# Kernel tuning notes

Hardware: AMD Instinct MI355X
Metric: run time of the kernel (lower is better)

Reference implementation:

```python
import jax, jax.numpy as jnp
from jax import lax
import numpy as np

BOX_SIZE = 64      # box_size
KERNEL = 5         # maxpool kernel (pad=2, stride=1)
THRESH = 0.95
MAX_BOXES = 256    # fixed-shape cap replacing torch nonzero()
NEG = -1e30        # padding value standing in for 'outside the image'


def setup_inputs() -> dict:
    key = jax.random.key(0)
    k1, k2 = jax.random.split(key)
    category_grids = jax.random.uniform(k1, (8, 3, 256, 256), dtype=jnp.float32)
    images = jax.random.normal(k2, (8, 3, 1024, 1024), dtype=jnp.float32)
    return {"category_grids": category_grids, "images": images}


def _maxpool_same(x):
    # nn.MaxPool2d(kernel_size=5, padding=2, stride=1)
    return lax.reduce_window(x, -jnp.inf, lax.max,
                             (1, 1, KERNEL, KERNEL), (1, 1, 1, 1), 'SAME')


def reference(category_grids, images):
    B, C, Hg, Wg = category_grids.shape
    # ---- GridsToBoxes: maxpool-equality peak NMS + threshold ----
    is_peak = (_maxpool_same(category_grids) == category_grids) & (category_grids > THRESH)
    peaks = category_grids * is_peak  # zero everywhere except peaks

    # fixed-shape replacement for nonzero(): per-image top-k over (C*Hg*Wg)
    flat = peaks.reshape(B, -1)
    vals, idx = lax.top_k(flat, MAX_BOXES)          # [B, K]
    valid = vals > 0.0                              # peak values are > THRESH > 0
    rem = idx % (Hg * Wg)
    cy = rem // Wg                                  # [B, K] int32
    cx = rem % Wg

    half = BOX_SIZE // 2
    x1 = cx - half
    y1 = cy - half
    # box_convert cxcywh -> xyxy
    boxes = jnp.stack([x1, y1, cx + half, cy + half], axis=-1).astype(jnp.float32)  # [B,K,4]

    # ---- CenterCrop: roi_pool(images, boxes, output_size=BOX_SIZE) ----
    # torchvision roi_pool: roi_width = x2-x1+1 = BOX_SIZE+1, adaptive max-pooled to BOX_SIZE bins;
    # out-of-image bins give 0. Emulate by padding with NEG and max-gathering fixed bins.
    P = BOX_SIZE + 1
    pad = BOX_SIZE
    padded = jnp.pad(images, ((0, 0), (0, 0), (pad, pad), (pad, pad)),
                     constant_values=NEG)

    def crop_one(img, y, x):  # img: [3, Hp, Wp]
        return lax.dynamic_slice(img, (0, y + pad, x + pad), (img.shape[0], P, P))

    patches = jax.vmap(lambda img, ys, xs:
                       jax.vmap(lambda y, x: crop_one(img, y, x))(ys, xs)
                       )(padded, y1, x1)            # [B, K, 3, P, P]

    # static adaptive-maxpool bin boundaries: bin i covers [floor(i*P/O), ceil((i+1)*P/O))
    O = BOX_SIZE
    i = np.arange(O)
    b0 = np.floor(i * P / O).astype(np.int32)       # bin width is 1 or 2 -> two gathers suffice
    b1 = (np.ceil((i + 1) * P / O) - 1).astype(np.int32)
    rows = jnp.maximum(patches[..., b0, :], patches[..., b1, :])   # pool H: [B,K,3,O,P]
    pooled = jnp.maximum(rows[..., b0], rows[..., b1])             # pool W: [B,K,3,O,O]
    pooled = jnp.where(pooled < NEG * 0.5, 0.0, pooled)            # empty/outside bins -> 0
    pooled = pooled * valid[:, :, None, None, None].astype(pooled.dtype)

    return peaks, boxes, pooled, valid
```

## Files before the change

kernel.cpp:

```cpp
#include <hip/hip_runtime.h>
#include <stdint.h>
#include <math.h>

#define NB 8
#define NC 3
#define HG 256
#define WG 256
#define IMG 1024
#define TOPK 256
#define HALF 32
#define PEAK_THRESH 0.95f
#define NEGV (-1e30f)
#define SELCAP 2048
#define VB_LO 0x3F733334u
#define NBUCK 256
#define BSHIFT 12

#define ROWS_PB 16
#define GRPS (HG / ROWS_PB)
#define PLANES (NB * NC)
#define PK_BLOCKS (PLANES * GRPS)
#define SLOTS 256

#define PROWS 65
#define PQUADS 17
#define PSTRIDE 76

typedef float f32x4 __attribute__((ext_vector_type(4)));

#define WS_BCAND_OFF 4096
#define WS_SEL_OFF   (WS_BCAND_OFF + (size_t)PK_BLOCKS * SLOTS * 8)

__global__ void __launch_bounds__(256) peaks_kernel(const float* __restrict__ g,
                                                    float* __restrict__ peaks_out,
                                                    uint32_t* __restrict__ bcnt,
                                                    unsigned long long* __restrict__ bcand) {
    __shared__ float vms[ROWS_PB][WG];
    __shared__ unsigned long long lkeys[SLOTS];
    __shared__ uint32_t lcount;

    int blk   = blockIdx.x;
    int grp   = blk & (GRPS - 1);
    int plane = blk >> 4;
    int c     = plane % NC;
    int y0    = grp * ROWS_PB;
    int x     = threadIdx.x;

    if (x == 0) lcount = 0;

    const float* gc = g + (size_t)plane * (HG * WG);
    float col[ROWS_PB + 4];
#pragma unroll
    for (int d = 0; d < ROWS_PB + 4; ++d) {
        int yy = y0 - 2 + d;
        col[d] = (yy >= 0 && yy < HG) ? gc[yy * WG + x] : -INFINITY;
    }
#pragma unroll
    for (int r = 0; r < ROWS_PB; ++r)
        vms[r][x] = fmaxf(fmaxf(fmaxf(col[r], col[r + 1]), fmaxf(col[r + 2], col[r + 3])),
                          col[r + 4]);
    __syncthreads();

#pragma unroll
    for (int r = 0; r < ROWS_PB; ++r) {
        float v = col[r + 2];
        float h = vms[r][x];
        if (x >= 2)      h = fmaxf(h, vms[r][x - 2]);
        if (x >= 1)      h = fmaxf(h, vms[r][x - 1]);
        if (x <= WG - 2) h = fmaxf(h, vms[r][x + 1]);
        if (x <= WG - 3) h = fmaxf(h, vms[r][x + 2]);
        bool peak = (h == v) && (v > PEAK_THRESH);
        peaks_out[(size_t)plane * (HG * WG) + (y0 + r) * WG + x] = peak ? v : 0.0f;
        if (peak) {
            uint32_t pos = atomicAdd(&lcount, 1u);
            if (pos < SLOTS) {
                int cell = c * (HG * WG) + (y0 + r) * WG + x;
                lkeys[pos] = ((unsigned long long)__float_as_uint(v) << 32) |
                             (uint32_t)(~(uint32_t)cell);
            }
        }
    }
    __syncthreads();
    uint32_t n = min(lcount, (uint32_t)SLOTS);
    if (x == 0) bcnt[blk] = n;
    if ((uint32_t)x < n) bcand[(size_t)blk * SLOTS + x] = lkeys[x];
}

__device__ __forceinline__ void emit_entry(int b, int kk, int idx, int vld,
                                           float* boxes_out, float* valid_out, int4* sel) {
    int rem = idx & 65535;
    int cy = rem >> 8, cx = rem & 255;
    int x1 = cx - HALF, y1 = cy - HALF;
    float4 bo = make_float4((float)x1, (float)y1, (float)(cx + HALF), (float)(cy + HALF));
    *(float4*)(boxes_out + ((size_t)b * TOPK + kk) * 4) = bo;
    valid_out[b * TOPK + kk] = vld ? 1.0f : 0.0f;
    sel[b * TOPK + kk] = make_int4(y1, x1, vld, 0);
}

#define BLKS_PER_IMG (NC * GRPS)

__global__ void __launch_bounds__(1024) topk_kernel(const uint32_t* __restrict__ bcnt,
                                                    const unsigned long long* __restrict__ bcand,
                                                    float* __restrict__ boxes_out,
                                                    float* __restrict__ valid_out,
                                                    int4* __restrict__ sel) {
    __shared__ uint32_t hist[NBUCK];
    __shared__ uint32_t scnts[BLKS_PER_IMG];
    __shared__ unsigned long long skeys[SELCAP];
    __shared__ uint32_t sT, scnt;
    int b = blockIdx.x, t = threadIdx.x;

    if (t < NBUCK) hist[t] = 0;
    if (t < BLKS_PER_IMG) scnts[t] = bcnt[b * BLKS_PER_IMG + t];
    if (t == 0) { sT = 0; scnt = 0; }
    __syncthreads();

    const unsigned long long* cb = bcand + (size_t)b * BLKS_PER_IMG * SLOTS;

    for (int s = t; s < BLKS_PER_IMG * SLOTS; s += 1024) {
        int j = s >> 8, i = s & (SLOTS - 1);
        if ((uint32_t)i < scnts[j]) {
            uint32_t vb = (uint32_t)(cb[(size_t)j * SLOTS + i] >> 32);
            uint32_t bk = (vb - VB_LO) >> BSHIFT;
            if (bk > (NBUCK - 1u)) bk = NBUCK - 1u;
            atomicAdd(&hist[bk], 1u);
        }
    }
    __syncthreads();

    for (int off = 1; off < NBUCK; off <<= 1) {
        uint32_t v = 0;
        if (t < NBUCK) v = hist[t] + ((t + off < NBUCK) ? hist[t + off] : 0u);
        __syncthreads();
        if (t < NBUCK) hist[t] = v;
        __syncthreads();
    }
    if (t < NBUCK) {
        uint32_t st  = hist[t];
        uint32_t stn = (t < NBUCK - 1) ? hist[t + 1] : 0u;
        if (st >= TOPK && stn < TOPK) sT = (uint32_t)t;
    }
    __syncthreads();
    uint32_t T = sT;

    for (int s = t; s < BLKS_PER_IMG * SLOTS; s += 1024) {
        int j = s >> 8, i = s & (SLOTS - 1);
        if ((uint32_t)i < scnts[j]) {
            unsigned long long key = cb[(size_t)j * SLOTS + i];
            uint32_t vb = (uint32_t)(key >> 32);
            uint32_t bk = (vb - VB_LO) >> BSHIFT;
            if (bk > (NBUCK - 1u)) bk = NBUCK - 1u;
            if (bk >= T) {
                uint32_t p = atomicAdd(&scnt, 1u);
                if (p < SELCAP) skeys[p] = key;
            }
        }
    }
    __syncthreads();
    int nsel = (int)min(scnt, (uint32_t)SELCAP);

    if (nsel < TOPK && t < TOPK)
        emit_entry(b, t, t, 0, boxes_out, valid_out, sel);
    __syncthreads();

    for (int p = t; p < nsel; p += 1024) {
        unsigned long long key = skeys[p];
        int rank = 0;
        for (int i = 0; i < nsel; ++i)
            rank += (skeys[i] > key) ? 1 : 0;
        if (rank < TOPK)
            emit_entry(b, rank, (int)(~(uint32_t)key), 1, boxes_out, valid_out, sel);
    }
}

__global__ void __launch_bounds__(256) crop_kernel(const float* __restrict__ images,
                                                   const int4* __restrict__ sel,
                                                   float* __restrict__ pooled) {
    __shared__ float patch[PROWS * PSTRIDE];

    int bk = blockIdx.x;
    int b  = bk >> 8;
    int4 s = sel[bk];
    int y1 = s.x, x1 = s.y, vld = s.z;

    int t  = threadIdx.x;
    int j0 = (t & 15) * 4;
    int rb = t >> 4;
    int xa = x1 & ~3;
    int c0 = x1 & 3;
    bool fast = (x1 >= 0 && y1 >= 0);

    for (int c = 0; c < NC; ++c) {
        const float* img  = images + ((size_t)b * NC + c) * (size_t)(IMG * IMG);
        float*       outc = pooled + ((size_t)bk * NC + c) * 4096;

        if (fast) {
            const float* p0 = img + (size_t)y1 * IMG + xa;
            for (int i = t; i < PROWS * PQUADS; i += 256) {
                int row = i / PQUADS, q = i - row * PQUADS;
                f32x4 v = *(const f32x4*)(p0 + (size_t)row * IMG + q * 4);
                *(f32x4*)(&patch[row * PSTRIDE + q * 4]) = v;
            }
        } else {
            for (int i = t; i < PROWS * PQUADS; i += 256) {
                int row = i / PQUADS, q = i - row * PQUADS;
                int yy = y1 + row;
                const float* rowp = img + (size_t)yy * IMG;
                f32x4 v;
#pragma unroll
                for (int e = 0; e < 4; ++e) {
                    int xx = xa + q * 4 + e;
                    v[e] = (yy >= 0 && xx >= 0) ? rowp[xx] : NEGV;
                }
                *(f32x4*)(&patch[row * PSTRIDE + q * 4]) = v;
            }
        }
        __syncthreads();

        float Y[5][8];
#pragma unroll
        for (int i = 0; i < 5; ++i) {
            f32x4 lo = *(const f32x4*)(&patch[(rb * 4 + i) * PSTRIDE + j0]);
            f32x4 hi = *(const f32x4*)(&patch[(rb * 4 + i) * PSTRIDE + j0 + 4]);
#pragma unroll
            for (int e = 0; e < 4; ++e) { Y[i][e] = lo[e]; Y[i][e + 4] = hi[e]; }
        }
#pragma unroll
        for (int it = 0; it < 4; ++it) {
            float w[8];
#pragma unroll
            for (int k = 0; k < 8; ++k) w[k] = fmaxf(Y[it][k], Y[it + 1][k]);
            f32x4 o;
#define DO_C0(C0) { _Pragma("unroll") for (int e = 0; e < 4; ++e) o[e] = fmaxf(w[(C0) + e], w[(C0) + e + 1]); }
            switch (c0) {
                case 0: DO_C0(0); break;
                case 1: DO_C0(1); break;
                case 2: DO_C0(2); break;
                default: DO_C0(3); break;
            }
#undef DO_C0
#pragma unroll
            for (int e = 0; e < 4; ++e) {
                float rr = o[e];
                if (!fast) rr = (rr < NEGV * 0.5f) ? 0.0f : rr;
                if (!vld) rr = 0.0f;
                o[e] = rr;
            }
            *(f32x4*)(outc + (rb * 4 + it) * 64 + j0) = o;
        }
        __syncthreads();
    }
}

extern "C" void kernel_launch(void* const* d_in, const int* in_sizes, int n_in,
                              void* d_out, int out_size, void* d_ws, size_t ws_size,
                              hipStream_t stream) {
    const float* grids  = (const float*)d_in[0];
    const float* images = (const float*)d_in[1];

    float* out = (float*)d_out;
    float* peaks_out = out;
    float* boxes_out = out + (size_t)NB * NC * HG * WG;
    float* pooled_out = boxes_out + (size_t)NB * TOPK * 4;
    float* valid_out = pooled_out + (size_t)NB * TOPK * NC * 64 * 64;

    uint32_t* bcnt = (uint32_t*)d_ws;
    unsigned long long* bcand = (unsigned long long*)((char*)d_ws + WS_BCAND_OFF);
    int4* sel = (int4*)((char*)d_ws + WS_SEL_OFF);

    peaks_kernel<<<PK_BLOCKS, 256, 0, stream>>>(grids, peaks_out, bcnt, bcand);

    topk_kernel<<<NB, 1024, 0, stream>>>(bcnt, bcand, boxes_out, valid_out, sel);

    crop_kernel<<<NB * TOPK, 256, 0, stream>>>(images, sel, pooled_out);
}
```

Measured before the change: 54.57 us.

## Reorder crop blocks by spatial location for image cache locality

```diff
diff --git a/kernel.cpp b/kernel.cpp
--- a/kernel.cpp
+++ b/kernel.cpp
@@ -30,6 +30,7 @@
 
 #define WS_BCAND_OFF 4096
 #define WS_SEL_OFF   (WS_BCAND_OFF + (size_t)PK_BLOCKS * SLOTS * 8)
+#define WS_ORD_OFF   (WS_SEL_OFF + (size_t)NB * TOPK * 16)
 
 __global__ void __launch_bounds__(256) peaks_kernel(const float* __restrict__ g,
                                                     float* __restrict__ peaks_out,
@@ -103,10 +104,12 @@
                                                     const unsigned long long* __restrict__ bcand,
                                                     float* __restrict__ boxes_out,
                                                     float* __restrict__ valid_out,
-                                                    int4* __restrict__ sel) {
+                                                    int4* __restrict__ sel,
+                                                    uint32_t* __restrict__ order_out) {
     __shared__ uint32_t hist[NBUCK];
     __shared__ uint32_t scnts[BLKS_PER_IMG];
     __shared__ unsigned long long skeys[SELCAP];
+    __shared__ uint32_t cell_by_rank[TOPK];
     __shared__ uint32_t sT, scnt;
     int b = blockIdx.x, t = threadIdx.x;
 
@@ -159,8 +162,10 @@
     __syncthreads();
     int nsel = (int)min(scnt, (uint32_t)SELCAP);
 
-    if (nsel < TOPK && t < TOPK)
+    if (nsel < TOPK && t < TOPK) {
         emit_entry(b, t, t, 0, boxes_out, valid_out, sel);
+        cell_by_rank[t] = (uint32_t)t;
+    }
     __syncthreads();
 
     for (int p = t; p < nsel; p += 1024) {
@@ -168,18 +173,38 @@
         int rank = 0;
         for (int i = 0; i < nsel; ++i)
             rank += (skeys[i] > key) ? 1 : 0;
-        if (rank < TOPK)
-            emit_entry(b, rank, (int)(~(uint32_t)key), 1, boxes_out, valid_out, sel);
+        if (rank < TOPK) {
+            int idx = (int)(~(uint32_t)key);
+            emit_entry(b, rank, idx, 1, boxes_out, valid_out, sel);
+            cell_by_rank[rank] = (uint32_t)idx;
+        }
+    }
+    __syncthreads();
+
+    if (t < TOPK) {
+        uint32_t cell = cell_by_rank[t];
+        uint32_t sk = ((cell & 0xFFFFu) << 2) | (cell >> 16);
+        int sr = 0;
+        for (int i = 0; i < TOPK; ++i) {
+            uint32_t ci = cell_by_rank[i];
+            uint32_t si = ((ci & 0xFFFFu) << 2) | (ci >> 16);
+            sr += (si < sk) ? 1 : 0;
+        }
+        order_out[b * TOPK + sr] = (uint32_t)t;
     }
 }
 
 __global__ void __launch_bounds__(256) crop_kernel(const float* __restrict__ images,
                                                    const int4* __restrict__ sel,
+                                                   const uint32_t* __restrict__ order,
                                                    float* __restrict__ pooled) {
     __shared__ float patch[PROWS * PSTRIDE];
 
-    int bk = blockIdx.x;
-    int b  = bk >> 8;
+    int bid  = blockIdx.x;
+    int b    = bid & 7;
+    int slot = bid >> 3;
+    int rank = (int)order[b * TOPK + slot];
+    int bk   = b * TOPK + rank;
     int4 s = sel[bk];
     int y1 = s.x, x1 = s.y, vld = s.z;
 
@@ -267,10 +292,11 @@
     uint32_t* bcnt = (uint32_t*)d_ws;
     unsigned long long* bcand = (unsigned long long*)((char*)d_ws + WS_BCAND_OFF);
     int4* sel = (int4*)((char*)d_ws + WS_SEL_OFF);
+    uint32_t* order = (uint32_t*)((char*)d_ws + WS_ORD_OFF);
 
     peaks_kernel<<<PK_BLOCKS, 256, 0, stream>>>(grids, peaks_out, bcnt, bcand);
 
-    topk_kernel<<<NB, 1024, 0, stream>>>(bcnt, bcand, boxes_out, valid_out, sel);
-
-    crop_kernel<<<NB * TOPK, 256, 0, stream>>>(images, sel, pooled_out);
-}
+    topk_kernel<<<NB, 1024, 0, stream>>>(bcnt, bcand, boxes_out, valid_out, sel, order);
+
+    crop_kernel<<<NB * TOPK, 256, 0, stream>>>(images, sel, order, pooled_out);
+}
```

Measured after the change: 51.82 us. 5.0% less time.
